# Optimization experiments

Hardware: AMD Instinct MI355X
Metric: run time of the kernel (lower is better)

Reference implementation:

```python
import jax, jax.numpy as jnp
import numpy as np
import math

H, G, DQK, DV = 16, 4, 64, 128  # n_head, n_kv_group, qk head dim, v head dim


def _rope(t):
    # t: [B, n, T, d] -- standard rotate-half RoPE, base 10000
    B, n, T, d = t.shape
    inv = 1.0 / (10000.0 ** (jnp.arange(0, d, 2, dtype=jnp.float32) / d))  # [d/2]
    ang = jnp.arange(T, dtype=jnp.float32)[:, None] * inv[None, :]          # [T, d/2]
    cos = jnp.concatenate([jnp.cos(ang), jnp.cos(ang)], axis=-1)            # [T, d]
    sin = jnp.concatenate([jnp.sin(ang), jnp.sin(ang)], axis=-1)
    t1, t2 = jnp.split(t, 2, axis=-1)
    rot = jnp.concatenate([-t2, t1], axis=-1)
    return t * cos + rot * sin


def setup_inputs() -> dict:
    key = jax.random.key(0)
    ks = jax.random.split(key, 6)
    B, T, C = 2, 2048, 1024
    x = jax.random.normal(ks[0], (B, T, C), jnp.float32)
    Wq = jax.random.normal(ks[1], (C, H * DQK), jnp.float32) * 0.02
    Wk = jax.random.normal(ks[2], (C, G * DQK), jnp.float32) * 0.02
    Wv = jax.random.normal(ks[3], (C, G * DV), jnp.float32) * 0.02
    Wproj = jax.random.normal(ks[4], (DV, C), jnp.float32) * 0.02
    lobo = jnp.full((H,), 1.0, jnp.float32)  # flash_lobo_log_const per head
    g0 = math.log2(T * T - T)                # qk_norm_factor init from block_size
    qk_norm_factor = jnp.array([g0], dtype=jnp.float32)
    return {"x": x, "iter_num": 0, "Wq": Wq, "Wk": Wk, "Wv": Wv,
            "Wproj": Wproj, "lobo": lobo, "qk_norm_factor": qk_norm_factor}


def reference(x, iter_num, Wq, Wk, Wv, Wproj, lobo, qk_norm_factor):
    B, T, C = x.shape
    # projections (bias=False)
    q = (x @ Wq).reshape(B, T, H, DQK).transpose(0, 2, 1, 3)   # [B,H,T,dqk]
    k = (x @ Wk).reshape(B, T, G, DQK).transpose(0, 2, 1, 3)   # [B,G,T,dqk]
    v = (x @ Wv).reshape(B, T, G, DV).transpose(0, 2, 1, 3)    # [B,G,T,dv]
    # rotary embeddings on q and k
    q = _rope(q)
    k = _rope(k)
    # qk-norm
    q = q / (jnp.linalg.norm(q, axis=-1, keepdims=True) + 1e-6)
    k = k / (jnp.linalg.norm(k, axis=-1, keepdims=True) + 1e-6)
    # learned logit scale: q *= g*sqrt(d), SDPA divides by sqrt(d) -> net scale g
    q = q * (qk_norm_factor[0] * jnp.sqrt(jnp.float32(DQK)))
    # GQA broadcast (repeat_interleave over kv groups)
    rep = H // G
    k = jnp.repeat(k, rep, axis=1)   # [B,H,T,dqk]
    v = jnp.repeat(v, rep, axis=1)   # [B,H,T,dv]
    logits = jnp.einsum('bhqd,bhkd->bhqk', q, k) / jnp.sqrt(jnp.float32(DQK))
    causal = jnp.tril(jnp.ones((T, T), dtype=bool))
    logits = jnp.where(causal[None, None], logits, -jnp.inf)
    # flash-lobo: zero-valued sink key, always visible, logit = per-head bias
    sink = jnp.broadcast_to(lobo[None, :, None, None], (B, H, T, 1))
    att = jax.nn.softmax(jnp.concatenate([sink, logits], axis=-1), axis=-1)
    y = jnp.einsum('bhqk,bhkd->bhqd', att[..., 1:], v)  # sink value is zero
    y = y.sum(axis=1)                                    # head-SUM merge [B,T,dv]
    return y @ Wproj                                     # [B,T,C]
```

## Files before the change

kernel.cpp:

```cpp
#include <hip/hip_runtime.h>
#include <hip/hip_bf16.h>
#include <math.h>

#define B_ 2
#define T_ 2048
#define C_ 1024
#define H_ 16
#define G_ 4
#define DQK_ 64
#define DV_ 128
#define NQKV 1792
#define KS2 2048

typedef __attribute__((ext_vector_type(8))) short short8;
typedef __attribute__((ext_vector_type(4))) float f32x4;
typedef unsigned short ushort_t;

__device__ inline ushort_t f2bf(float f) {
  union { float f; unsigned int u; } v; v.f = f;
  unsigned int r = (v.u + 0x7FFFu + ((v.u >> 16) & 1u)) >> 16;
  return (ushort_t)r;
}
__device__ inline float bf2f(ushort_t h) {
  union { unsigned int u; float f; } v; v.u = ((unsigned int)h) << 16;
  return v.f;
}
__device__ inline ushort_t f2bf_hw(float f) {
  unsigned int u;
  asm("v_cvt_pk_bf16_f32 %0, %1, %1" : "=v"(u) : "v"(f));
  return (ushort_t)u;
}

#define GLD_LDS16(g, l)                                              \
  __builtin_amdgcn_global_load_lds(                                  \
      (const __attribute__((address_space(1))) void*)(g),            \
      (__attribute__((address_space(3))) void*)(l), 16, 0, 0)

__global__ __launch_bounds__(256) void prep(
    const float* __restrict__ x, const float* __restrict__ Wq,
    const float* __restrict__ Wk, const float* __restrict__ Wv,
    const float* __restrict__ Wproj, ushort_t* __restrict__ xb,
    ushort_t* __restrict__ wt, ushort_t* __restrict__ wpf,
    float* __restrict__ y) {
  __shared__ float tile[64][65];
  const int bid = blockIdx.x;
  const int tid = threadIdx.x;

  if (bid < 2048) {
    int idx = bid * 256 + tid;
    int m = idx >> 7;
    int c8 = idx & 127;
    const float* src = &x[(size_t)m * 1024 + c8 * 8];
    float4 v0 = *(const float4*)&src[0];
    float4 v1 = *(const float4*)&src[4];
    float f[8] = {v0.x, v0.y, v0.z, v0.w, v1.x, v1.y, v1.z, v1.w};
    short8 hv, lv;
#pragma unroll
    for (int c = 0; c < 8; c++) {
      ushort_t h = f2bf(f[c]);
      hv[c] = (short)h;
      lv[c] = (short)f2bf(f[c] - bf2f(h));
    }
    int key = (m >> 1) & 3;
    int phys = (c8 & ~3) * 8 + ((c8 & 3) ^ key) * 8;
    ushort_t* row = xb + (size_t)m * KS2;
    *(short8*)&row[phys] = hv;
    *(short8*)&row[1024 + phys] = lv;
  } else if (bid < 2496) {
    const int wid = bid - 2048;
    const int n0 = (wid % 28) * 64;
    const int k0 = (wid / 28) * 64;

    const float* Wp; int ldw, noff;
    if (n0 < 1024)      { Wp = Wq; ldw = 1024; noff = n0; }
    else if (n0 < 1280) { Wp = Wk; ldw = 256;  noff = n0 - 1024; }
    else                { Wp = Wv; ldw = 512;  noff = n0 - 1280; }

#pragma unroll
    for (int it = 0; it < 4; it++) {
      int fi = it * 256 + tid;
      int kk = fi >> 4;
      int nc = (fi & 15) * 4;
      float4 v = *(const float4*)&Wp[(size_t)(k0 + kk) * ldw + noff + nc];
      tile[nc + 0][kk] = v.x; tile[nc + 1][kk] = v.y;
      tile[nc + 2][kk] = v.z; tile[nc + 3][kk] = v.w;
    }
    __syncthreads();
    int nn = tid >> 2, seg = tid & 3;
    int n = n0 + nn;
    int key = (n >> 1) & 3;
    ushort_t* row = wt + (size_t)n * KS2;
#pragma unroll
    for (int j = 0; j < 2; j++) {
      short8 hv;
#pragma unroll
      for (int u = 0; u < 8; u++)
        hv[u] = (short)f2bf(tile[nn][seg * 16 + j * 8 + u]);
      int c8 = (k0 >> 3) + seg * 2 + j;
      int phys = (c8 & ~3) * 8 + ((c8 & 3) ^ key) * 8;
      *(short8*)&row[phys] = hv;
    }
  } else if (bid < 2560) {
    int idx = (bid - 2496) * 256 + tid;
    int n = idx & 1023;
    int kc = idx >> 10;
    short8 v;
#pragma unroll
    for (int j = 0; j < 8; j++)
      v[j] = (short)f2bf(Wproj[(size_t)(kc * 8 + j) * 1024 + n]);
    size_t off = (((size_t)(n >> 7) * 4 + (kc >> 2)) * 8 + ((n >> 4) & 7)) * 512 +
                 ((kc & 3) * 16 + (n & 15)) * 8;
    *(short8*)&wpf[off] = v;
  } else {
    int idx = (bid - 2560) * 256 + tid;
    *(float4*)&y[(size_t)idx * 4] = (float4){0.f, 0.f, 0.f, 0.f};
  }
}

__global__ __launch_bounds__(256) void gemm_qkv_mfma(
    const ushort_t* __restrict__ xb, const ushort_t* __restrict__ wt,
    ushort_t* __restrict__ qf, ushort_t* __restrict__ kf,
    ushort_t* __restrict__ vf) {
  __shared__ ushort_t At[128 * 64];
  __shared__ ushort_t Bt[128 * 64];
  const int tid = threadIdx.x;
  const int wave = tid >> 6, lane = tid & 63;
  const int quad = lane >> 4, l16 = lane & 15;
  const int m0 = blockIdx.y * 128, n0 = blockIdx.x * 128;
  const int wm = (wave & 1) * 64, wn = (wave >> 1) * 64;
  const int key = (l16 >> 1) & 3;
  const int ntiles = (n0 >= 1280) ? 16 : 32;

  f32x4 acc[4][4];
#pragma unroll
  for (int i = 0; i < 4; i++)
#pragma unroll
    for (int j = 0; j < 4; j++) acc[i][j] = (f32x4){0.f, 0.f, 0.f, 0.f};

  const int rA = wave * 32 + (lane >> 3);
  const int cA = (lane & 7) * 8;
  const ushort_t* gA = xb + (size_t)(m0 + rA) * KS2 + cA;
  const ushort_t* gB = wt + (size_t)(n0 + rA) * KS2 + cA;

  for (int kt = 0; kt < ntiles; kt++) {
    const int ca = kt * 64;
    const int cb = (kt < 16 ? kt : kt - 16) * 64;
    __syncthreads();
#pragma unroll
    for (int j = 0; j < 4; j++) {
      GLD_LDS16(gA + ca + (size_t)(8 * j) * KS2, &At[(wave * 32 + 8 * j) * 64]);
      GLD_LDS16(gB + cb + (size_t)(8 * j) * KS2, &Bt[(wave * 32 + 8 * j) * 64]);
    }
    __syncthreads();

#pragma unroll
    for (int s = 0; s < 2; s++) {
      const int off = s * 32 + ((quad ^ key) * 8);
      short8 af[4], bf[4];
#pragma unroll
      for (int i = 0; i < 4; i++)
        af[i] = *(const short8*)&At[(wm + 16 * i + l16) * 64 + off];
#pragma unroll
      for (int j = 0; j < 4; j++)
        bf[j] = *(const short8*)&Bt[(wn + 16 * j + l16) * 64 + off];
#pragma unroll
      for (int i = 0; i < 4; i++)
#pragma unroll
        for (int j = 0; j < 4; j++)
          acc[i][j] = __builtin_amdgcn_mfma_f32_16x16x32_bf16(
              af[i], bf[j], acc[i][j], 0, 0, 0);
    }
  }

  const int b = m0 >> 11;

  if (n0 >= 1280) {
    const int g = (n0 - 1280) >> 7;
    ushort_t* vg = vf + (size_t)(b * 4 + g) * 262144;
#pragma unroll
    for (int i = 0; i < 4; i++) {
      int mbase = m0 + wm + 16 * i + quad * 4;
#pragma unroll
      for (int jn = 0; jn < 4; jn++) {
        int nv = (wn >> 4) + jn;
#pragma unroll
        for (int r = 0; r < 4; r++) {
          int t = (mbase + r) & 2047;
          int tk = t >> 6, ks = (t >> 5) & 1, qd = (t >> 3) & 3, jj = t & 7;
          size_t off = ((size_t)(tk * 16 + ks * 8 + nv) * 4 + qd) * 128 +
                       l16 * 8 + jj;
          vg[off] = f2bf(acc[i][jn][r]);
        }
      }
    }
  } else {
    const int headn = n0 + wn;
    const bool isq = headn < 1024;
    ushort_t* dstbase = isq
        ? qf + (size_t)(b * 16 + (headn >> 6)) * 131072
        : kf + (size_t)(b * 4 + ((headn - 1024) >> 6)) * 131072;
    const float c0 = 0.4152410118074239f;
    const float inv_lo = exp2f(-(float)l16 * c0);
    const float inv_hi = exp2f(-(float)(16 + l16) * c0);
    const int jj = l16 & 7;

#pragma unroll
    for (int i = 0; i < 4; i++) {
#pragma unroll
      for (int r = 0; r < 4; r++) {
        int t = (m0 + wm + 16 * i + quad * 4 + r) & 2047;
        float sn0, cs0, sn1, cs1;
        __sincosf((float)t * inv_lo, &sn0, &cs0);
        __sincosf((float)t * inv_hi, &sn1, &cs1);
        float rv0 = acc[i][0][r] * cs0 - acc[i][2][r] * sn0;
        float rv1 = acc[i][1][r] * cs1 - acc[i][3][r] * sn1;
        float rv2 = acc[i][2][r] * cs0 + acc[i][0][r] * sn0;
        float rv3 = acc[i][3][r] * cs1 + acc[i][1][r] * sn1;
        float ss = rv0 * rv0 + rv1 * rv1 + rv2 * rv2 + rv3 * rv3;
        ss += __shfl_xor(ss, 1, 64);
        ss += __shfl_xor(ss, 2, 64);
        ss += __shfl_xor(ss, 4, 64);
        ss += __shfl_xor(ss, 8, 64);
        float sc = 1.0f / (sqrtf(ss) + 1e-6f);
        int kt8 = t >> 6, tt = t & 63;
        int l16v = tt & 15, nt = tt >> 4;
        float rv[4] = {rv0, rv1, rv2, rv3};
#pragma unroll
        for (int j = 0; j < 4; j++) {
          int ks = j >> 1;
          int qd = (2 * j + (l16 >> 3)) & 3;
          size_t idx512 = isq ? (size_t)(kt8 * 8 + nt * 2 + ks)
                              : (size_t)(kt8 * 8 + ks * 4 + nt);
          dstbase[idx512 * 512 + qd * 128 + l16v * 8 + jj] = f2bf(rv[j] * sc);
        }
      }
    }
  }
}

__global__ __launch_bounds__(256, 4) void attn(
    const ushort_t* __restrict__ qf, const ushort_t* __restrict__ kf,
    const ushort_t* __restrict__ vf, const float* __restrict__ lobo,
    const float* __restrict__ qknf, float* __restrict__ y) {
  const int f = blockIdx.x;
  const int bh = f & 31;
  const int slot = f >> 5;
  int tq;
  if (slot < 8)       tq = 31 - slot;
  else if (slot < 16) tq = 8 + slot;
  else if (slot < 24) tq = 31 - slot;
  else                tq = slot - 24;
  const int b = bh >> 4;
  const int h = bh & 15;
  const int g = h >> 2;

  __shared__ ushort_t KV[12288];
  __shared__ ushort_t Ps[4 * 1088];

  const int tid = threadIdx.x;
  const int wave = tid >> 6, lane = tid & 63;
  const int quad = lane >> 4, l16 = lane & 15;
  ushort_t* PsW = &Ps[wave * 1088];

  short8 bones;
  {
    short bv = (l16 == 0) ? (short)0x3F80 : (short)0;
#pragma unroll
    for (int j = 0; j < 8; j++) bones[j] = bv;
  }

  const ushort_t* qbase = qf + (size_t)(b * 16 + h) * 131072 + lane * 8;
  short8 aq0 = *(const short8*)&qbase[(size_t)(tq * 8 + wave * 2 + 0) * 512];
  short8 aq1 = *(const short8*)&qbase[(size_t)(tq * 8 + wave * 2 + 1) * 512];

  f32x4 o[9];
#pragma unroll
  for (int nv = 0; nv < 9; nv++) o[nv] = (f32x4){0.f, 0.f, 0.f, 0.f};

  const float gsc = qknf[0];
  const float sinkp = __expf(lobo[h] - gsc);

  const int row = tq * 64 + wave * 16 + quad * 4;

  const ushort_t* kgl = kf + (size_t)(b * 4 + g) * 131072 + lane * 8;
  const ushort_t* vgl = vf + (size_t)(b * 4 + g) * 262144 + lane * 8;

  for (int kt = 0; kt <= tq; kt++) {
    __syncthreads();
    {
      const ushort_t* gk = kgl + (size_t)kt * 4096;
      const ushort_t* gv = vgl + (size_t)kt * 8192;
      GLD_LDS16(gk + (wave * 2 + 0) * 512, &KV[(wave * 2 + 0) * 512]);
      GLD_LDS16(gk + (wave * 2 + 1) * 512, &KV[(wave * 2 + 1) * 512]);
#pragma unroll
      for (int j = 0; j < 4; j++)
        GLD_LDS16(gv + (wave * 4 + j) * 512, &KV[4096 + (wave * 4 + j) * 512]);
    }
    __syncthreads();

    f32x4 s[4];
#pragma unroll
    for (int nt = 0; nt < 4; nt++) s[nt] = (f32x4){0.f, 0.f, 0.f, 0.f};
    {
      short8 kb[4];
#pragma unroll
      for (int u = 0; u < 4; u++)
        kb[u] = *(const short8*)&KV[u * 512 + lane * 8];
      __builtin_amdgcn_s_setprio(1);
#pragma unroll
      for (int nt = 0; nt < 4; nt++)
        s[nt] = __builtin_amdgcn_mfma_f32_16x16x32_bf16(aq0, kb[nt], s[nt], 0, 0, 0);
      __builtin_amdgcn_s_setprio(0);
#pragma unroll
      for (int u = 0; u < 4; u++)
        kb[u] = *(const short8*)&KV[(4 + u) * 512 + lane * 8];
      __builtin_amdgcn_s_setprio(1);
#pragma unroll
      for (int nt = 0; nt < 4; nt++)
        s[nt] = __builtin_amdgcn_mfma_f32_16x16x32_bf16(aq1, kb[nt], s[nt], 0, 0, 0);
      __builtin_amdgcn_s_setprio(0);
    }

    if (kt == tq) {
#pragma unroll
      for (int nt = 0; nt < 4; nt++) {
        int key = kt * 64 + l16 + nt * 16;
#pragma unroll
        for (int r = 0; r < 4; r++) {
          float pv = (key <= row + r) ? __expf(fmaf(s[nt][r], gsc, -gsc)) : 0.f;
          PsW[(quad * 4 + r) * 68 + nt * 16 + l16] = f2bf_hw(pv);
        }
      }
    } else {
#pragma unroll
      for (int nt = 0; nt < 4; nt++)
#pragma unroll
        for (int r = 0; r < 4; r++)
          PsW[(quad * 4 + r) * 68 + nt * 16 + l16] =
              f2bf_hw(__expf(fmaf(s[nt][r], gsc, -gsc)));
    }

    short8 ap0 = *(const short8*)&PsW[l16 * 68 + quad * 8];
    short8 ap1 = *(const short8*)&PsW[l16 * 68 + 32 + quad * 8];
    {
      short8 vb[4];
#pragma unroll
      for (int u = 0; u < 4; u++)
        vb[u] = *(const short8*)&KV[4096 + u * 512 + lane * 8];
      __builtin_amdgcn_s_setprio(1);
#pragma unroll
      for (int nv = 0; nv < 4; nv++)
        o[nv] = __builtin_amdgcn_mfma_f32_16x16x32_bf16(ap0, vb[nv], o[nv], 0, 0, 0);
      __builtin_amdgcn_s_setprio(0);
#pragma unroll
      for (int u = 0; u < 4; u++)
        vb[u] = *(const short8*)&KV[4096 + (4 + u) * 512 + lane * 8];
      __builtin_amdgcn_s_setprio(1);
#pragma unroll
      for (int nv = 0; nv < 4; nv++)
        o[4 + nv] = __builtin_amdgcn_mfma_f32_16x16x32_bf16(ap0, vb[nv], o[4 + nv], 0, 0, 0);
      o[8] = __builtin_amdgcn_mfma_f32_16x16x32_bf16(ap0, bones, o[8], 0, 0, 0);
      o[8] = __builtin_amdgcn_mfma_f32_16x16x32_bf16(ap1, bones, o[8], 0, 0, 0);
      __builtin_amdgcn_s_setprio(0);
#pragma unroll
      for (int u = 0; u < 4; u++)
        vb[u] = *(const short8*)&KV[4096 + (8 + u) * 512 + lane * 8];
      __builtin_amdgcn_s_setprio(1);
#pragma unroll
      for (int nv = 0; nv < 4; nv++)
        o[nv] = __builtin_amdgcn_mfma_f32_16x16x32_bf16(ap1, vb[nv], o[nv], 0, 0, 0);
      __builtin_amdgcn_s_setprio(0);
#pragma unroll
      for (int u = 0; u < 4; u++)
        vb[u] = *(const short8*)&KV[4096 + (12 + u) * 512 + lane * 8];
      __builtin_amdgcn_s_setprio(1);
#pragma unroll
      for (int nv = 0; nv < 4; nv++)
        o[4 + nv] = __builtin_amdgcn_mfma_f32_16x16x32_bf16(ap1, vb[nv], o[4 + nv], 0, 0, 0);
      __builtin_amdgcn_s_setprio(0);
    }
  }

#pragma unroll
  for (int r = 0; r < 4; r++) {
    float lm = __shfl(o[8][r], lane & 48, 64);
    float invl = 1.0f / (lm + sinkp);
    size_t gRow = (size_t)b * T_ + row + r;
#pragma unroll
    for (int nv = 0; nv < 8; nv++)
      atomicAdd(&y[gRow * 128 + nv * 16 + l16], o[nv][r] * invl);
  }
}

__global__ __launch_bounds__(256) void out_proj(
    const float* __restrict__ y, const ushort_t* __restrict__ wpf,
    float* __restrict__ out) {
  __shared__ ushort_t yl[128 * 136];
  const int tid = threadIdx.x;
  const int wave = tid >> 6, lane = tid & 63;
  const int quad = lane >> 4, l16 = lane & 15;
  const int n0 = blockIdx.x * 128, m0 = blockIdx.y * 128;
  const int wm = (wave & 1) * 64, wn = (wave >> 1) * 64;

#pragma unroll
  for (int it = 0; it < 8; it++) {
    int p = it * 256 + tid;
    int row = p >> 4, c8 = p & 15;
    const float* src = &y[(size_t)(m0 + row) * 128 + c8 * 8];
    float4 v0 = *(const float4*)&src[0];
    float4 v1 = *(const float4*)&src[4];
    float fv[8] = {v0.x, v0.y, v0.z, v0.w, v1.x, v1.y, v1.z, v1.w};
    short8 hv;
#pragma unroll
    for (int c = 0; c < 8; c++) hv[c] = (short)f2bf(fv[c]);
    *(short8*)&yl[row * 136 + c8 * 8] = hv;
  }
  __syncthreads();

  f32x4 acc[4][4];
#pragma unroll
  for (int i = 0; i < 4; i++)
#pragma unroll
    for (int j = 0; j < 4; j++) acc[i][j] = (f32x4){0.f, 0.f, 0.f, 0.f};

#pragma unroll
  for (int ks = 0; ks < 4; ks++) {
    short8 af[4], bfr[4];
#pragma unroll
    for (int i = 0; i < 4; i++)
      af[i] = *(const short8*)&yl[(wm + 16 * i + l16) * 136 + (ks * 4 + quad) * 8];
    const ushort_t* wb = wpf + (((size_t)(n0 >> 7) * 4 + ks) * 8) * 512;
#pragma unroll
    for (int j = 0; j < 4; j++)
      bfr[j] = *(const short8*)&wb[((size_t)((wn >> 4) + j)) * 512 + lane * 8];
#pragma unroll
    for (int i = 0; i < 4; i++)
#pragma unroll
      for (int j = 0; j < 4; j++)
        acc[i][j] = __builtin_amdgcn_mfma_f32_16x16x32_bf16(
            af[i], bfr[j], acc[i][j], 0, 0, 0);
  }

#pragma unroll
  for (int i = 0; i < 4; i++) {
    int m = m0 + wm + 16 * i + quad * 4;
#pragma unroll
    for (int j = 0; j < 4; j++) {
      int n = n0 + wn + 16 * j + l16;
#pragma unroll
      for (int r = 0; r < 4; r++)
        out[(size_t)(m + r) * 1024 + n] = acc[i][j][r];
    }
  }
}

extern "C" void kernel_launch(void* const* d_in, const int* in_sizes, int n_in,
                              void* d_out, int out_size, void* d_ws, size_t ws_size,
                              hipStream_t stream) {
  const float* x     = (const float*)d_in[0];
  const float* Wq    = (const float*)d_in[2];
  const float* Wk    = (const float*)d_in[3];
  const float* Wv    = (const float*)d_in[4];
  const float* Wproj = (const float*)d_in[5];
  const float* lobo  = (const float*)d_in[6];
  const float* qknf  = (const float*)d_in[7];
  float* out = (float*)d_out;

  ushort_t* qf = (ushort_t*)d_ws;
  ushort_t* kf = qf + (size_t)B_ * H_ * T_ * 64;
  ushort_t* vf = kf + (size_t)B_ * G_ * T_ * 64;
  float* y = (float*)(vf + (size_t)B_ * G_ * T_ * 128);
  ushort_t* xb = (ushort_t*)((float*)d_ws + (size_t)B_ * T_ * NQKV);
  ushort_t* wt = xb + (size_t)B_ * T_ * KS2;
  ushort_t* wpf = wt + (size_t)NQKV * KS2;

  prep<<<3072, 256, 0, stream>>>(x, Wq, Wk, Wv, Wproj, xb, wt, wpf, y);

  dim3 gg(NQKV / 128, (B_ * T_) / 128);
  gemm_qkv_mfma<<<gg, 256, 0, stream>>>(xb, wt, qf, kf, vf);

  attn<<<B_ * H_ * 32, 256, 0, stream>>>(qf, kf, vf, lobo, qknf, y);

  dim3 go(8, 32);
  out_proj<<<go, 256, 0, stream>>>(y, wpf, out);
}
```

Before: 195.9 us.

## Prefetch next K/V tile into registers during attention compute

Replaces the direct global-to-LDS K/V loads at the top of each key-tile iteration with register-staged prefetching. The next tile is loaded into registers before the current tile's MFMA work, then written to LDS between two barriers at the end of the iteration. This is meant to hide global load latency behind compute, at the cost of 24 more VGPRs per thread for staging and extra LDS store instructions, which may lower occupancy.

```diff
diff --git a/kernel.cpp b/kernel.cpp
--- a/kernel.cpp
+++ b/kernel.cpp
@@ -282,21 +282,37 @@
 
   const int row = tq * 64 + wave * 16 + quad * 4;
 
-  const ushort_t* kgl = kf + (size_t)(b * 4 + g) * 131072 + lane * 8;
-  const ushort_t* vgl = vf + (size_t)(b * 4 + g) * 262144 + lane * 8;
+  const ushort_t* kbase = kf + (size_t)(b * 4 + g) * 131072;
+  const ushort_t* vbase = vf + (size_t)(b * 4 + g) * 262144;
+
+  short8 st0, st1, st2, st3, st4, st5;
+#define LOAD_TILE(ktv)                                                    \
+  {                                                                       \
+    const ushort_t* kq = kbase + (size_t)(ktv) * 4096;                    \
+    const ushort_t* vq = vbase + (size_t)(ktv) * 8192;                    \
+    st0 = *(const short8*)&kq[tid * 8];                                   \
+    st1 = *(const short8*)&kq[(256 + tid) * 8];                           \
+    st2 = *(const short8*)&vq[tid * 8];                                   \
+    st3 = *(const short8*)&vq[(256 + tid) * 8];                           \
+    st4 = *(const short8*)&vq[(512 + tid) * 8];                           \
+    st5 = *(const short8*)&vq[(768 + tid) * 8];                           \
+  }
+#define WRITE_TILE()                                                      \
+  {                                                                       \
+    *(short8*)&KV[tid * 8] = st0;                                         \
+    *(short8*)&KV[(256 + tid) * 8] = st1;                                 \
+    *(short8*)&KV[4096 + tid * 8] = st2;                                  \
+    *(short8*)&KV[4096 + (256 + tid) * 8] = st3;                          \
+    *(short8*)&KV[4096 + (512 + tid) * 8] = st4;                          \
+    *(short8*)&KV[4096 + (768 + tid) * 8] = st5;                          \
+  }
+
+  LOAD_TILE(0);
+  WRITE_TILE();
+  __syncthreads();
 
   for (int kt = 0; kt <= tq; kt++) {
-    __syncthreads();
-    {
-      const ushort_t* gk = kgl + (size_t)kt * 4096;
-      const ushort_t* gv = vgl + (size_t)kt * 8192;
-      GLD_LDS16(gk + (wave * 2 + 0) * 512, &KV[(wave * 2 + 0) * 512]);
-      GLD_LDS16(gk + (wave * 2 + 1) * 512, &KV[(wave * 2 + 1) * 512]);
-#pragma unroll
-      for (int j = 0; j < 4; j++)
-        GLD_LDS16(gv + (wave * 4 + j) * 512, &KV[4096 + (wave * 4 + j) * 512]);
-    }
-    __syncthreads();
+    if (kt < tq) LOAD_TILE(kt + 1);
 
     f32x4 s[4];
 #pragma unroll
@@ -379,6 +395,12 @@
         o[4 + nv] = __builtin_amdgcn_mfma_f32_16x16x32_bf16(ap1, vb[nv], o[4 + nv], 0, 0, 0);
       __builtin_amdgcn_s_setprio(0);
     }
+
+    if (kt < tq) {
+      __syncthreads();
+      WRITE_TILE();
+      __syncthreads();
+    }
   }
 
 #pragma unroll
@@ -390,6 +412,8 @@
     for (int nv = 0; nv < 8; nv++)
       atomicAdd(&y[gRow * 128 + nv * 16 + l16], o[nv][r] * invl);
   }
+#undef LOAD_TILE
+#undef WRITE_TILE
 }
 
 __global__ __launch_bounds__(256) void out_proj(
```

New measurement: 201.6 us. 2.9% more time.
